# Kernel tuning notes

Hardware: AMD Instinct MI355X
Metric: run time of the kernel (lower is better)

## Reference

```python
import jax, jax.numpy as jnp
import numpy as np
from jax import lax

# Mamba2 block (training path: mamba_split_conv1d_scan_combined equivalent)
B = 2; L = 2048; D_MODEL = 2048
INTER = 4096          # ssm_intermediate_size
NH = 64; HD = INTER // NH   # num_heads, head_dim
N = 128               # ssm_state_size
G = 1                 # n_groups
K = 4                 # conv kernel
CS = 256              # chunk size
EPS = 1e-5
CONV_DIM = INTER + 2 * G * N          # 4352
PROJ_DIM = INTER + CONV_DIM + NH      # 8512


def setup_inputs() -> dict:
    key = jax.random.key(0)
    ks = jax.random.split(key, 4)
    std = 0.02
    return {
        "hidden_states": jax.random.normal(ks[0], (B, L, D_MODEL), jnp.float32),
        "W_in": jax.random.normal(ks[1], (PROJ_DIM, D_MODEL), jnp.float32) * std,
        "conv_w": jax.random.normal(ks[2], (CONV_DIM, K), jnp.float32) * std,
        "conv_b": jnp.zeros((CONV_DIM,), jnp.float32),
        "dt_bias": jnp.ones((NH,), jnp.float32),
        "A_log": jnp.log(jnp.arange(1, NH + 1, dtype=jnp.float32)),
        "D": jnp.ones((NH,), jnp.float32),
        "norm_w": jnp.ones((INTER,), jnp.float32),
        "W_out": jax.random.normal(ks[3], (D_MODEL, INTER), jnp.float32) * std,
    }


def _segsum(x):
    # x: [..., s] -> [..., s, s] lower-triangular cumulative sums (masked with -inf)
    s = x.shape[-1]
    xc = jnp.cumsum(x, axis=-1)
    d = xc[..., :, None] - xc[..., None, :]
    return jnp.where(jnp.tril(jnp.ones((s, s), dtype=bool)), d, -jnp.inf)


def _forward(hidden_states, W_in, conv_w, conv_b, dt_bias, A_log, D, norm_w, W_out):
    proj = hidden_states @ W_in.T                              # [B,L,PROJ_DIM]
    gate = proj[..., :INTER]
    hBC = proj[..., INTER:INTER + CONV_DIM]
    dt = proj[..., INTER + CONV_DIM:]                          # [B,L,NH]

    # causal depthwise conv1d + silu
    xc = hBC.transpose(0, 2, 1)                                # [B,CONV_DIM,L]
    y = lax.conv_general_dilated(
        xc, conv_w[:, None, :], (1,), [(K - 1, 0)],
        dimension_numbers=("NCH", "OIH", "NCH"), feature_group_count=CONV_DIM)
    hBC = jax.nn.silu(y + conv_b[None, :, None]).transpose(0, 2, 1)

    x = hBC[..., :INTER].reshape(B, L, NH, HD)
    Bm = hBC[..., INTER:INTER + G * N].reshape(B, L, G, N)
    Cm = hBC[..., INTER + G * N:].reshape(B, L, G, N)

    dtv = jax.nn.softplus(dt + dt_bias)                        # [B,L,NH], dt_softplus=True
    A = -jnp.exp(A_log)                                        # [NH]

    # ---- chunked selective scan (SSD) ----
    c = L // CS
    xch = x.reshape(B, c, CS, NH, HD)
    dtch = dtv.reshape(B, c, CS, NH)
    Bh = jnp.repeat(Bm.reshape(B, c, CS, G, N), NH // G, axis=3)   # [B,c,s,NH,N]
    Ch = jnp.repeat(Cm.reshape(B, c, CS, G, N), NH // G, axis=3)

    dA = (dtch * A).transpose(0, 3, 1, 2)                      # [B,NH,c,s]
    Acum = jnp.cumsum(dA, axis=-1)                             # [B,NH,c,s]
    Lmat = jnp.exp(_segsum(dA))                                # [B,NH,c,s,s]

    # within-chunk (diagonal block) output
    Ydiag = jnp.einsum("bcihn,bcjhn,bhcij,bcjh,bcjhp->bcihp",
                       Ch, Bh, Lmat, dtch, xch)

    # per-chunk states
    decay_states = jnp.exp(Acum[..., -1:] - Acum)              # [B,NH,c,s]
    states = jnp.einsum("bcjhn,bhcj,bcjh,bcjhp->bchpn",
                        Bh, decay_states, dtch, xch)           # [B,c,NH,HD,N]

    # inter-chunk recurrence (scan over chunks)
    chunk_decay = jnp.exp(Acum[..., -1])                       # [B,NH,c]

    def step(carry, inp):
        st, dec = inp
        new = dec[:, :, None, None] * carry + st
        return new, carry                                      # emit state at chunk start

    init = jnp.zeros((B, NH, HD, N), dtype=x.dtype)
    _, prev = lax.scan(step, init,
                       (states.transpose(1, 0, 2, 3, 4), chunk_decay.transpose(2, 0, 1)))
    prev = prev.transpose(1, 0, 2, 3, 4)                       # [B,c,NH,HD,N]

    Yoff = jnp.einsum("bcihn,bchpn,bhci->bcihp", Ch, prev, jnp.exp(Acum))

    Y = (Ydiag + Yoff).reshape(B, L, NH, HD) + x * D[None, None, :, None]
    yout = Y.reshape(B, L, INTER)

    # gated RMSNorm (norm_before_gate=False): gate first, then normalize
    yout = yout * jax.nn.silu(gate)
    yout = yout * lax.rsqrt(jnp.mean(yout * yout, axis=-1, keepdims=True) + EPS) * norm_w
    return yout @ W_out.T                                      # [B,L,D_MODEL]


def reference(hidden_states, W_in, conv_w, conv_b, dt_bias, A_log, D, norm_w, W_out):
    return _forward(hidden_states, W_in, conv_w, conv_b, dt_bias, A_log, D, norm_w, W_out)
```

## Files before the change

kernel.cpp:

```cpp
#include <hip/hip_runtime.h>
#include <cstdint>

typedef __bf16 bf16;
typedef __bf16 bf16x8 __attribute__((ext_vector_type(8)));
typedef __bf16 bf16x4 __attribute__((ext_vector_type(4)));
typedef float  f32x4  __attribute__((ext_vector_type(4)));

#define BQ     2
#define LQ     2048
#define DMODEL 2048
#define INTER  4096
#define NH     64
#define HD     64
#define NS     128
#define CS     256
#define NC     8
#define CONVD  4352
#define PROJD  8512
#define PROJP  8576
#define PROJW  8704
#define MTOT   4096
#define EPSF   1e-5f
#define LOG2E  1.44269504088896f

__device__ __forceinline__ void async_ld16(const bf16* g, bf16* l) {
  __builtin_amdgcn_global_load_lds(
      (__attribute__((address_space(1))) void*)(uintptr_t)g,
      (__attribute__((address_space(3))) void*)l, 16, 0, 0);
}

__device__ __forceinline__ float siluf(float x) { return x / (1.f + expf(-x)); }

#define SB()    __builtin_amdgcn_sched_barrier(0)
#define HWBAR() __builtin_amdgcn_s_barrier()
#define LGKM0() asm volatile("s_waitcnt lgkmcnt(0)" ::: "memory")

__global__ void cast4_k(const float* __restrict__ in, bf16* __restrict__ out, long n4) {
  long i = (long)blockIdx.x * 256 + threadIdx.x;
  if (i >= n4) return;
  float4 v = ((const float4*)in)[i];
  bf16x4 o; o[0] = (bf16)v.x; o[1] = (bf16)v.y; o[2] = (bf16)v.z; o[3] = (bf16)v.w;
  ((bf16x4*)out)[i] = o;
}

__global__ void cast_pad_win_k(const float* __restrict__ W, bf16* __restrict__ out) {
  long i = (long)blockIdx.x * 256 + threadIdx.x;
  long tot = (long)PROJW * (DMODEL / 4);
  if (i >= tot) return;
  long row = i / (DMODEL / 4);
  long k4  = i % (DMODEL / 4);
  bf16x4 o;
  if (row < PROJD) {
    float4 v = ((const float4*)W)[row * (DMODEL / 4) + k4];
    o[0] = (bf16)v.x; o[1] = (bf16)v.y; o[2] = (bf16)v.z; o[3] = (bf16)v.w;
  } else {
    o[0] = o[1] = o[2] = o[3] = (bf16)0.f;
  }
  ((bf16x4*)out)[i] = o;
}


template<int R0>
__device__ __forceinline__ void ldB4(bf16x8 (&dst)[4][2], const char* base,
                                     int r16, int quad, int xr) {
  #pragma unroll
  for (int f = 0; f < 4; ++f)
    #pragma unroll
    for (int kk = 0; kk < 2; ++kk)
      dst[f][kk] = *(const bf16x8*)(base + (((R0 + f) * 16 + r16) << 7)
                                         + ((((kk << 2) + quad) ^ xr) << 4));
}

template<int R0>
__device__ __forceinline__ void ldA4(bf16x8 (&dst)[8][2], const char* base,
                                     int r16, int quad, int xr) {
  #pragma unroll
  for (int f = 0; f < 4; ++f)
    #pragma unroll
    for (int kk = 0; kk < 2; ++kk)
      dst[R0 + f][kk] = *(const bf16x8*)(base + (((R0 + f) * 16 + r16) << 7)
                                              + ((((kk << 2) + quad) ^ xr) << 4));
}

template<int MH, int NHALF>
__device__ __forceinline__ void qmfma(f32x4 (&acc)[8][4], const bf16x8 (&a)[8][2],
                                      const bf16x8 (&b)[4][2]) {
  #pragma unroll
  for (int kk = 0; kk < 2; ++kk)
    #pragma unroll
    for (int nf = 0; nf < 2; ++nf)
      #pragma unroll
      for (int mm = 0; mm < 4; ++mm)
        acc[MH * 4 + mm][NHALF * 2 + nf] = __builtin_amdgcn_mfma_f32_16x16x32_bf16(
            a[MH * 4 + mm][kk], b[NHALF * 2 + nf][kk], acc[MH * 4 + mm][NHALF * 2 + nf], 0, 0, 0);
}

__global__ __launch_bounds__(512, 2) void gemm8(
    const bf16* __restrict__ A, const bf16* __restrict__ W,
    bf16* __restrict__ Cb, float* __restrict__ Cf,
    int M, int Nn, int Ntiles, int K, int KS, int outf32)
{
  __shared__ int4 lds4[8192];
  char* lds = (char*)lds4;
  const int tid  = threadIdx.x;
  const int w    = tid >> 6;
  const int l    = tid & 63;
  const int wm   = w >> 2;
  const int wn   = w & 3;
  const int quad = l >> 4;
  const int r16  = l & 15;
  const int xr   = r16 & 7;

  const int Mtiles  = M >> 8;
  const int tilesMN = Mtiles * Ntiles;
  const int nwg = tilesMN * KS;
  int bid = blockIdx.x;
  int sid = ((nwg & 7) == 0) ? ((bid & 7) * (nwg >> 3) + (bid >> 3)) : bid;
  const int ks  = sid / tilesMN;
  const int rem = sid - ks * tilesMN;
  const int by = rem % Mtiles;
  const int bx = rem / Mtiles;
  const long tm = (long)by << 8;
  const long tn = (long)bx << 8;
  const int  NT = K / (64 * KS);
  const long kbase = (long)ks * (K / KS);

  const int srow = w * 8 + (l >> 3);
  const int scg  = (l & 7) ^ ((l >> 3) & 7);
  const bf16* Ab = A + (tm + srow) * K + kbase + scg * 8;
  const bf16* Wb = W + (tn + srow) * K + kbase + scg * 8;

  auto stage = [&](int tile, int part) {
    if (tile < NT) {
      const bf16* s = (part < 2 ? Ab : Wb) + (long)((part & 1) * 128) * K + (long)tile * 64;
      char* d = lds + ((tile & 1) << 16) + (part << 14) + (w << 10);
      async_ld16(s, (bf16*)d);
      async_ld16(s + (long)K * 64, (bf16*)(d + 8192));
    }
  };

  stage(0, 0); stage(0, 1); stage(0, 2); stage(0, 3);
  stage(1, 2); stage(1, 3); stage(1, 0);
  asm volatile("s_waitcnt vmcnt(6)" ::: "memory");
  SB();
  HWBAR();

  f32x4 acc[8][4] = {};

  for (int T = 0; T < NT; ++T) {
    const int bsel = (T & 1) << 16;
    const char* as = lds + bsel + (wm << 14);
    const char* bs = lds + bsel + 32768 + ((wn >> 1) << 14) + ((wn & 1) << 13);
    bf16x8 a[8][2], b[4][2];

    ldB4<0>(b, bs, r16, quad, xr);
    ldA4<0>(a, as, r16, quad, xr);
    stage(T + 1, 1);
    HWBAR(); LGKM0(); SB();
    __builtin_amdgcn_s_setprio(1);
    qmfma<0, 0>(acc, a, b);
    __builtin_amdgcn_s_setprio(0);
    HWBAR();

    ldA4<4>(a, as, r16, quad, xr);
    stage(T + 2, 2);
    HWBAR(); LGKM0(); SB();
    __builtin_amdgcn_s_setprio(1);
    qmfma<1, 0>(acc, a, b);
    __builtin_amdgcn_s_setprio(0);
    HWBAR();

    stage(T + 2, 3);
    HWBAR();
    __builtin_amdgcn_s_setprio(1);
    qmfma<0, 1>(acc, a, b);
    __builtin_amdgcn_s_setprio(0);
    HWBAR();

    stage(T + 2, 0);
    HWBAR();
    __builtin_amdgcn_s_setprio(1);
    qmfma<1, 1>(acc, a, b);
    __builtin_amdgcn_s_setprio(0);
    if (T + 2 < NT) { asm volatile("s_waitcnt vmcnt(6)" ::: "memory"); }
    else            { asm volatile("s_waitcnt vmcnt(0)" ::: "memory"); }
    SB();
    HWBAR();
  }

  const long cbase = (long)ks * M * Nn;
  #pragma unroll
  for (int mf = 0; mf < 8; ++mf)
    #pragma unroll
    for (int nf = 0; nf < 4; ++nf) {
      long r0 = tm + wm * 128 + mf * 16 + quad * 4;
      long cc = tn + wn * 64 + nf * 16 + r16;
      if (cc < Nn) {
        #pragma unroll
        for (int reg = 0; reg < 4; ++reg) {
          long idx = (r0 + reg) * (long)Nn + cc;
          if (outf32) Cf[cbase + idx] = acc[mf][nf][reg];
          else        Cb[idx] = (bf16)acc[mf][nf][reg];
        }
      }
    }
}

__global__ void addred_k(const float* __restrict__ P, float* __restrict__ out, long n4) {
  long i = (long)blockIdx.x * 256 + threadIdx.x;
  if (i >= n4) return;
  float4 a = ((const float4*)P)[i];
  float4 b = ((const float4*)P)[i + n4];
  float4 r; r.x = a.x + b.x; r.y = a.y + b.y; r.z = a.z + b.z; r.w = a.w + b.w;
  ((float4*)out)[i] = r;
}

__global__ void conv_silu_k(const bf16* __restrict__ proj,
                            const float* __restrict__ conv_w,
                            const float* __restrict__ conv_b,
                            bf16* __restrict__ xconv,
                            bf16* __restrict__ Bmb, bf16* __restrict__ Cmb,
                            bf16* __restrict__ Bt)
{
  int ch = blockIdx.x * 256 + threadIdx.x;
  if (ch >= CONVD) return;
  long bl = blockIdx.y;
  int l = (int)(bl & (LQ - 1));
  float acc = conv_b[ch];
  #pragma unroll
  for (int t = 0; t < 4; ++t) {
    int ls = l - 3 + t;
    if (ls >= 0)
      acc += (float)proj[(bl - 3 + t) * PROJP + INTER + ch] * conv_w[ch * 4 + t];
  }
  float y = siluf(acc);
  if (ch < INTER) {
    xconv[bl * INTER + ch] = (bf16)y;
  } else if (ch < INTER + NS) {
    int n = ch - INTER;
    Bmb[bl * NS + n] = (bf16)y;
    int b = (int)(bl >> 11), ci = l >> 8, j = l & 255;
    Bt[(((long)(b * NC + ci) * NS) + n) * CS + j] = (bf16)y;
  } else {
    Cmb[bl * NS + (ch - INTER - NS)] = (bf16)y;
  }
}

__global__ __launch_bounds__(CS) void dt_prep_k(
    const bf16* __restrict__ proj, const float* __restrict__ dt_bias,
    const float* __restrict__ A_log,
    float* __restrict__ dtv, float* __restrict__ acum, float* __restrict__ cdec)
{
  int bx = blockIdx.x;
  int ci = bx & 7;
  int bh = bx >> 3;
  int h  = bh & 63;
  int b  = bh >> 6;
  int i  = threadIdx.x;
  long pos = (long)b * LQ + ci * CS + i;
  float draw = (float)proj[pos * PROJP + INTER + CONVD + h] + dt_bias[h];
  float dv = draw > 20.f ? draw : log1pf(expf(draw));
  float Ah = -expf(A_log[h]);
  __shared__ float s[CS];
  s[i] = dv * Ah;
  __syncthreads();
  for (int off = 1; off < CS; off <<= 1) {
    float t = (i >= off) ? s[i - off] : 0.f;
    __syncthreads();
    s[i] += t;
    __syncthreads();
  }
  long base = (long)bx * CS;
  dtv[base + i]  = dv;
  acum[base + i] = s[i];
  if (i == 0) cdec[bx] = expf(s[CS - 1]);
}

__global__ __launch_bounds__(256) void gmat_k(
    const bf16* __restrict__ Cmb, const bf16* __restrict__ Bmb, float* __restrict__ Gnt)
{
  int q  = blockIdx.x;
  int bc = blockIdx.y;
  long bl0 = (long)(bc >> 3) * LQ + (bc & 7) * CS;
  int wave = threadIdx.x >> 6, lane = threadIdx.x & 63;
  int quad = lane >> 4, r16 = lane & 15;
  int i0 = (q >> 1) * 128 + (wave >> 1) * 64;
  int j0 = (q & 1)  * 128 + (wave & 1)  * 64;

  f32x4 acc[4][4] = {};
  #pragma unroll
  for (int kt = 0; kt < 4; ++kt) {
    int k0 = kt * 32 + quad * 8;
    bf16x8 af[4], bfv[4];
    #pragma unroll
    for (int it = 0; it < 4; ++it)
      af[it] = *(const bf16x8*)&Cmb[(bl0 + i0 + it * 16 + r16) * NS + k0];
    #pragma unroll
    for (int nt = 0; nt < 4; ++nt)
      bfv[nt] = *(const bf16x8*)&Bmb[(bl0 + j0 + nt * 16 + r16) * NS + k0];
    #pragma unroll
    for (int it = 0; it < 4; ++it)
      #pragma unroll
      for (int nt = 0; nt < 4; ++nt)
        acc[it][nt] = __builtin_amdgcn_mfma_f32_16x16x32_bf16(af[it], bfv[nt], acc[it][nt], 0, 0, 0);
  }
  #pragma unroll
  for (int it = 0; it < 4; ++it)
    #pragma unroll
    for (int nt = 0; nt < 4; ++nt)
      #pragma unroll
      for (int reg = 0; reg < 4; ++reg) {
        int i = i0 + it * 16 + quad * 4 + reg;
        int j = j0 + nt * 16 + r16;
        Gnt[((long)bc * CS + i) * CS + j] = acc[it][nt][reg];
      }
}

__global__ __launch_bounds__(256) void states_k(
    const bf16* __restrict__ xconv, const bf16* __restrict__ Bt,
    const float* __restrict__ dtv, const float* __restrict__ acum,
    bf16* __restrict__ st)
{
  int bx = blockIdx.x;
  int h = bx & 63, bc = bx >> 6;
  int b = bc >> 3, ci = bc & 7;
  long bl0 = (long)b * LQ + ci * CS;
  long abase = ((long)(b * NH + h) * NC + ci) * CS;
  int t = threadIdx.x;
  int wave = t >> 6, lane = t & 63, quad = lane >> 4, r16 = lane & 15;

  __shared__ bf16 Xt[64][264];
  __shared__ float ws[CS];
  __shared__ float ac_s[CS];
  ac_s[t] = acum[abase + t];
  __syncthreads();
  float alast = ac_s[CS - 1];
  ws[t] = expf(alast - ac_s[t]) * dtv[abase + t];
  {
    int col = t & 63, grp = t >> 6;
    for (int r = 0; r < 64; ++r) {
      int j = grp * 64 + r;
      Xt[col][j] = xconv[(bl0 + j) * INTER + h * HD + col];
    }
  }
  __syncthreads();

  const bf16* btb = &Bt[(long)bc * NS * CS];
  f32x4 acc[8] = {};
  int p = wave * 16 + r16;
  #pragma unroll
  for (int kt = 0; kt < 8; ++kt) {
    int k0 = kt * 32 + quad * 8;
    bf16x8 xv = *(const bf16x8*)&Xt[p][k0];
    float w8[8];
    *(float4*)&w8[0] = *(const float4*)&ws[k0];
    *(float4*)&w8[4] = *(const float4*)&ws[k0 + 4];
    bf16x8 af;
    #pragma unroll
    for (int jj = 0; jj < 8; ++jj) af[jj] = (bf16)((float)xv[jj] * w8[jj]);
    #pragma unroll
    for (int nt = 0; nt < 8; ++nt) {
      bf16x8 bfv = *(const bf16x8*)&btb[(nt * 16 + r16) * CS + k0];
      acc[nt] = __builtin_amdgcn_mfma_f32_16x16x32_bf16(af, bfv, acc[nt], 0, 0, 0);
    }
  }
  #pragma unroll
  for (int nt = 0; nt < 8; ++nt)
    #pragma unroll
    for (int reg = 0; reg < 4; ++reg) {
      int prow = wave * 16 + quad * 4 + reg;
      int n = nt * 16 + r16;
      st[((long)bx * HD + prow) * NS + n] = (bf16)acc[nt][reg];
    }
}

__global__ void scan_k(bf16* __restrict__ st, const float* __restrict__ cdec)
{
  long t = (long)blockIdx.x * 256 + threadIdx.x;
  int n = (int)(t & 127);
  int p = (int)((t >> 7) & 63);
  int h = (int)((t >> 13) & 63);
  int b = (int)(t >> 19);
  float carry = 0.f;
  for (int ci = 0; ci < NC; ++ci) {
    long idx = (((long)(b * NC + ci) * NH + h) * HD + p) * NS + n;
    float v = (float)st[idx];
    st[idx] = (bf16)carry;
    carry = cdec[(b * NH + h) * NC + ci] * carry + v;
  }
}

#define XTP 392
__global__ __launch_bounds__(256) void ymix_k(
    const bf16* __restrict__ xconv, const float* __restrict__ Gnt,
    const bf16* __restrict__ prev, const bf16* __restrict__ Cmb,
    const float* __restrict__ dtv, const float* __restrict__ acum,
    const float* __restrict__ Dp, bf16* __restrict__ Y)
{
  int bx = blockIdx.x;
  int h = bx & 63, bc = bx >> 6;
  int b = bc >> 3, ci = bc & 7;
  long bl0 = (long)b * LQ + ci * CS;
  long abase = ((long)(b * NH + h) * NC + ci) * CS;
  int t = threadIdx.x;
  int wave = t >> 6, lane = t & 63;
  int quad = lane >> 4, r16 = lane & 15;
  int iw = wave * 64;

  __shared__ bf16 Xt[64][XTP];
  __shared__ float a2s[CS], dts[CS], eas[CS];

  {
    float ac = acum[abase + t];
    a2s[t] = ac * LOG2E;
    dts[t] = dtv[abase + t];
    eas[t] = expf(ac);
  }
  {
    int col = t & 63, grp = t >> 6;
    for (int r = 0; r < 64; ++r) {
      int j = grp * 64 + r;
      Xt[col][j] = xconv[(bl0 + j) * INTER + h * HD + col];
    }
  }
  for (int r = 0; r < 32; ++r) {
    int idx = t + r * 256;
    int n = idx & 127, p = idx >> 7;
    Xt[p][256 + n] = prev[((long)bx * HD + p) * NS + n];
  }
  __syncthreads();

  f32x4 acc[4][4] = {};

  for (int kt = 0; kt < 12; ++kt) {
    int k0 = kt * 32;
    bool cpart = (k0 >= 256);
    if (!cpart && k0 > iw + 63) continue;

    bf16x8 bfrag[4];
    #pragma unroll
    for (int nt = 0; nt < 4; ++nt)
      bfrag[nt] = *(const bf16x8*)&Xt[nt * 16 + r16][k0 + quad * 8];

    if (!cpart) {
      int j0 = k0 + quad * 8;
      float dt8[8], a28[8];
      *(float4*)&dt8[0] = *(const float4*)&dts[j0];
      *(float4*)&dt8[4] = *(const float4*)&dts[j0 + 4];
      *(float4*)&a28[0] = *(const float4*)&a2s[j0];
      *(float4*)&a28[4] = *(const float4*)&a2s[j0 + 4];
      #pragma unroll
      for (int it = 0; it < 4; ++it) {
        if (k0 > iw + it * 16 + 15) continue;
        int i = iw + it * 16 + r16;
        float a2i = a2s[i];
        const float* gp = &Gnt[((long)bc * CS + i) * CS + j0];
        float g[8];
        *(float4*)&g[0] = *(const float4*)gp;
        *(float4*)&g[4] = *(const float4*)(gp + 4);
        bf16x8 af;
        #pragma unroll
        for (int jj = 0; jj < 8; ++jj) {
          float v = g[jj] * dt8[jj] * exp2f(a2i - a28[jj]);
          v = (j0 + jj <= i) ? v : 0.f;
          af[jj] = (bf16)v;
        }
        #pragma unroll
        for (int nt = 0; nt < 4; ++nt)
          acc[it][nt] = __builtin_amdgcn_mfma_f32_16x16x32_bf16(af, bfrag[nt], acc[it][nt], 0, 0, 0);
      }
    } else {
      int n0 = k0 - 256 + quad * 8;
      #pragma unroll
      for (int it = 0; it < 4; ++it) {
        int i = iw + it * 16 + r16;
        float e = eas[i];
        bf16x8 cv = *(const bf16x8*)&Cmb[(bl0 + i) * NS + n0];
        bf16x8 af;
        #pragma unroll
        for (int jj = 0; jj < 8; ++jj)
          af[jj] = (bf16)(e * (float)cv[jj]);
        #pragma unroll
        for (int nt = 0; nt < 4; ++nt)
          acc[it][nt] = __builtin_amdgcn_mfma_f32_16x16x32_bf16(af, bfrag[nt], acc[it][nt], 0, 0, 0);
      }
    }
  }

  float Dh = Dp[h];
  #pragma unroll
  for (int it = 0; it < 4; ++it)
    #pragma unroll
    for (int nt = 0; nt < 4; ++nt) {
      int i0 = iw + it * 16 + quad * 4;
      int p  = nt * 16 + r16;
      bf16x4 xv = *(const bf16x4*)&Xt[p][i0];
      #pragma unroll
      for (int reg = 0; reg < 4; ++reg) {
        float v = acc[it][nt][reg] + Dh * (float)xv[reg];
        Y[(bl0 + i0 + reg) * INTER + h * HD + p] = (bf16)v;
      }
    }
}

__global__ __launch_bounds__(256) void norm_k(
    bf16* __restrict__ Y, const bf16* __restrict__ proj,
    const float* __restrict__ norm_w)
{
  long bl = blockIdx.x;
  int t = threadIdx.x;
  __shared__ float yb[INTER];
  __shared__ float red[256];
  float ss = 0.f;
  for (int r = 0; r < 16; ++r) {
    int ch = t + r * 256;
    float g = (float)proj[bl * PROJP + ch];
    float yv = (float)Y[bl * INTER + ch] * siluf(g);
    yb[ch] = yv;
    ss += yv * yv;
  }
  red[t] = ss;
  __syncthreads();
  for (int s = 128; s > 0; s >>= 1) {
    if (t < s) red[t] += red[t + s];
    __syncthreads();
  }
  float scale = rsqrtf(red[0] / (float)INTER + EPSF);
  for (int r = 0; r < 16; ++r) {
    int ch = t + r * 256;
    Y[bl * INTER + ch] = (bf16)(yb[ch] * scale * norm_w[ch]);
  }
}

extern "C" void kernel_launch(void* const* d_in, const int* in_sizes, int n_in,
                              void* d_out, int out_size, void* d_ws, size_t ws_size,
                              hipStream_t stream)
{
  (void)in_sizes; (void)n_in; (void)out_size; (void)ws_size;
  const float* hidden  = (const float*)d_in[0];
  const float* W_in    = (const float*)d_in[1];
  const float* conv_w  = (const float*)d_in[2];
  const float* conv_b  = (const float*)d_in[3];
  const float* dt_bias = (const float*)d_in[4];
  const float* A_log   = (const float*)d_in[5];
  const float* Dp      = (const float*)d_in[6];
  const float* norm_w  = (const float*)d_in[7];
  const float* W_out   = (const float*)d_in[8];
  float* out = (float*)d_out;

  char* ws    = (char*)d_ws;
  bf16* projb = (bf16*)(ws);
  char* base2 = ws + 70254592;
  bf16*  hb    = (bf16*)(base2);
  bf16*  winb  = (bf16*)(base2 + 16777216);
  bf16*  xconv = (bf16*)(base2);
  bf16*  st    = (bf16*)(base2 + 33554432);
  float* Gnt   = (float*)(base2 + 50331648);
  bf16*  Bmb   = (bf16*)(base2 + 54525952);
  bf16*  Cmb   = (bf16*)(base2 + 55574528);
  float* dtv   = (float*)(base2 + 56623104);
  float* acum  = (float*)(base2 + 57671680);
  float* cdec  = (float*)(base2 + 58720256);
  bf16*  Bt    = (bf16*)(base2 + 58724352);
  bf16*  Yb    = xconv;
  bf16*  woutb = st;

  cast4_k<<<dim3((unsigned)((MTOT * (long)DMODEL / 4 + 255) / 256)), 256, 0, stream>>>(
      hidden, hb, (long)MTOT * DMODEL / 4);
  cast_pad_win_k<<<dim3((unsigned)(((long)PROJW * (DMODEL / 4) + 255) / 256)), 256, 0, stream>>>(
      W_in, winb);
  gemm8<<<dim3((PROJW / 256) * (MTOT / 256)), 512, 0, stream>>>(
      hb, winb, projb, nullptr, MTOT, PROJP, PROJW / 256, DMODEL, 1, 0);

  conv_silu_k<<<dim3(CONVD / 256, MTOT), 256, 0, stream>>>(
      projb, conv_w, conv_b, xconv, Bmb, Cmb, Bt);
  dt_prep_k<<<dim3(BQ * NH * NC), CS, 0, stream>>>(
      projb, dt_bias, A_log, dtv, acum, cdec);
  gmat_k<<<dim3(4, BQ * NC), 256, 0, stream>>>(Cmb, Bmb, Gnt);
  states_k<<<dim3(BQ * NC * NH), 256, 0, stream>>>(xconv, Bt, dtv, acum, st);
  scan_k<<<dim3(BQ * NH * HD * NS / 256), 256, 0, stream>>>(st, cdec);
  ymix_k<<<dim3(BQ * NC * NH), 256, 0, stream>>>(
      xconv, Gnt, st, Cmb, dtv, acum, Dp, Yb);

  cast4_k<<<dim3((unsigned)((DMODEL * (long)INTER / 4 + 255) / 256)), 256, 0, stream>>>(
      W_out, woutb, (long)DMODEL * INTER / 4);
  norm_k<<<dim3(MTOT), 256, 0, stream>>>(Yb, projb, norm_w);
  gemm8<<<dim3((DMODEL / 256) * (MTOT / 256) * 2), 512, 0, stream>>>(
      Yb, woutb, nullptr, (float*)projb, MTOT, DMODEL, DMODEL / 256, INTER, 2, 1);
  addred_k<<<dim3((unsigned)((MTOT * (long)DMODEL / 4 + 255) / 256)), 256, 0, stream>>>(
      (const float*)projb, out, (long)MTOT * DMODEL / 4);
}
```

Baseline: 667.9 us.

## Restructure GEMM main loop into half-tile register double buffering; vectorize norm kernel

```diff
diff --git a/kernel.cpp b/kernel.cpp
--- a/kernel.cpp
+++ b/kernel.cpp
@@ -33,7 +33,6 @@
 
 #define SB()    __builtin_amdgcn_sched_barrier(0)
 #define HWBAR() __builtin_amdgcn_s_barrier()
-#define LGKM0() asm volatile("s_waitcnt lgkmcnt(0)" ::: "memory")
 
 __global__ void cast4_k(const float* __restrict__ in, bf16* __restrict__ out, long n4) {
   long i = (long)blockIdx.x * 256 + threadIdx.x;
@@ -60,39 +59,39 @@
 }
 
 
-template<int R0>
-__device__ __forceinline__ void ldB4(bf16x8 (&dst)[4][2], const char* base,
+template<int MH>
+__device__ __forceinline__ void ldAh(bf16x8 (&dst)[4][2], const char* base,
                                      int r16, int quad, int xr) {
   #pragma unroll
   for (int f = 0; f < 4; ++f)
     #pragma unroll
     for (int kk = 0; kk < 2; ++kk)
-      dst[f][kk] = *(const bf16x8*)(base + (((R0 + f) * 16 + r16) << 7)
+      dst[f][kk] = *(const bf16x8*)(base + ((((MH * 4 + f) * 16) + r16) << 7)
                                          + ((((kk << 2) + quad) ^ xr) << 4));
 }
 
-template<int R0>
-__device__ __forceinline__ void ldA4(bf16x8 (&dst)[8][2], const char* base,
+template<int NH2>
+__device__ __forceinline__ void ldBh(bf16x8 (&dst)[2][2], const char* base,
                                      int r16, int quad, int xr) {
   #pragma unroll
-  for (int f = 0; f < 4; ++f)
+  for (int f = 0; f < 2; ++f)
     #pragma unroll
     for (int kk = 0; kk < 2; ++kk)
-      dst[R0 + f][kk] = *(const bf16x8*)(base + (((R0 + f) * 16 + r16) << 7)
-                                              + ((((kk << 2) + quad) ^ xr) << 4));
-}
-
-template<int MH, int NHALF>
-__device__ __forceinline__ void qmfma(f32x4 (&acc)[8][4], const bf16x8 (&a)[8][2],
-                                      const bf16x8 (&b)[4][2]) {
+      dst[f][kk] = *(const bf16x8*)(base + ((((NH2 * 2 + f) * 16) + r16) << 7)
+                                         + ((((kk << 2) + quad) ^ xr) << 4));
+}
+
+template<int MH, int NH2>
+__device__ __forceinline__ void qmfma(f32x4 (&acc)[8][4], const bf16x8 (&a)[4][2],
+                                      const bf16x8 (&b)[2][2]) {
   #pragma unroll
   for (int kk = 0; kk < 2; ++kk)
     #pragma unroll
     for (int nf = 0; nf < 2; ++nf)
       #pragma unroll
       for (int mm = 0; mm < 4; ++mm)
-        acc[MH * 4 + mm][NHALF * 2 + nf] = __builtin_amdgcn_mfma_f32_16x16x32_bf16(
-            a[MH * 4 + mm][kk], b[NHALF * 2 + nf][kk], acc[MH * 4 + mm][NHALF * 2 + nf], 0, 0, 0);
+        acc[MH * 4 + mm][NH2 * 2 + nf] = __builtin_amdgcn_mfma_f32_16x16x32_bf16(
+            a[mm][kk], b[nf][kk], acc[MH * 4 + mm][NH2 * 2 + nf], 0, 0, 0);
 }
 
 __global__ __launch_bounds__(512, 2) void gemm8(
@@ -140,53 +139,56 @@
   };
 
   stage(0, 0); stage(0, 1); stage(0, 2); stage(0, 3);
-  stage(1, 2); stage(1, 3); stage(1, 0);
-  asm volatile("s_waitcnt vmcnt(6)" ::: "memory");
+  stage(1, 2); stage(1, 3);
+  asm volatile("s_waitcnt vmcnt(4)" ::: "memory");
   SB();
   HWBAR();
+  SB();
+
+  bf16x8 a0[4][2], a1[4][2], b0[2][2], b1[2][2];
+  {
+    const char* as0 = lds + (wm << 14);
+    const char* bs0 = lds + 32768 + ((wn >> 1) << 14) + ((wn & 1) << 13);
+    ldAh<0>(a0, as0, r16, quad, xr);
+    ldBh<0>(b0, bs0, r16, quad, xr);
+  }
 
   f32x4 acc[8][4] = {};
 
   for (int T = 0; T < NT; ++T) {
-    const int bsel = (T & 1) << 16;
-    const char* as = lds + bsel + (wm << 14);
-    const char* bs = lds + bsel + 32768 + ((wn >> 1) << 14) + ((wn & 1) << 13);
-    bf16x8 a[8][2], b[4][2];
-
-    ldB4<0>(b, bs, r16, quad, xr);
-    ldA4<0>(a, as, r16, quad, xr);
-    stage(T + 1, 1);
-    HWBAR(); LGKM0(); SB();
+    const int bsel  = (T & 1) << 16;
+    const char* as  = lds + bsel + (wm << 14);
+    const char* bs  = lds + bsel + 32768 + ((wn >> 1) << 14) + ((wn & 1) << 13);
+    const char* asN = lds + (bsel ^ 0x10000) + (wm << 14);
+    const char* bsN = lds + (bsel ^ 0x10000) + 32768 + ((wn >> 1) << 14) + ((wn & 1) << 13);
+
+    SB();
+    stage(T + 1, 0); stage(T + 1, 1);
+    ldBh<1>(b1, bs, r16, quad, xr);
+    ldAh<1>(a1, as, r16, quad, xr);
+    SB(); HWBAR(); SB();
+
     __builtin_amdgcn_s_setprio(1);
-    qmfma<0, 0>(acc, a, b);
+    qmfma<0, 0>(acc, a0, b0);
     __builtin_amdgcn_s_setprio(0);
-    HWBAR();
-
-    ldA4<4>(a, as, r16, quad, xr);
-    stage(T + 2, 2);
-    HWBAR(); LGKM0(); SB();
+    SB(); HWBAR(); SB();
+
     __builtin_amdgcn_s_setprio(1);
-    qmfma<1, 0>(acc, a, b);
+    qmfma<0, 1>(acc, a0, b1);
     __builtin_amdgcn_s_setprio(0);
-    HWBAR();
-
-    stage(T + 2, 3);
-    HWBAR();
+    asm volatile("s_waitcnt vmcnt(0)" ::: "memory");
+    SB(); HWBAR(); SB();
+
     __builtin_amdgcn_s_setprio(1);
-    qmfma<0, 1>(acc, a, b);
+    qmfma<1, 0>(acc, a1, b0);
+    qmfma<1, 1>(acc, a1, b1);
     __builtin_amdgcn_s_setprio(0);
-    HWBAR();
-
-    stage(T + 2, 0);
-    HWBAR();
-    __builtin_amdgcn_s_setprio(1);
-    qmfma<1, 1>(acc, a, b);
-    __builtin_amdgcn_s_setprio(0);
-    if (T + 2 < NT) { asm volatile("s_waitcnt vmcnt(6)" ::: "memory"); }
-    else            { asm volatile("s_waitcnt vmcnt(0)" ::: "memory"); }
-    SB();
-    HWBAR();
-  }
+    ldAh<0>(a0, asN, r16, quad, xr);
+    ldBh<0>(b0, bsN, r16, quad, xr);
+    stage(T + 2, 2); stage(T + 2, 3);
+    SB(); HWBAR();
+  }
+  asm volatile("s_waitcnt vmcnt(0)" ::: "memory");
 
   const long cbase = (long)ks * M * Nn;
   #pragma unroll
@@ -509,16 +511,31 @@
 {
   long bl = blockIdx.x;
   int t = threadIdx.x;
-  __shared__ float yb[INTER];
+  const bf16* yrow = Y + bl * INTER;
+  const bf16* grow = proj + bl * PROJP;
+  int c0 = t * 16;
+
+  bf16x8 y0 = *(const bf16x8*)&yrow[c0];
+  bf16x8 y1 = *(const bf16x8*)&yrow[c0 + 8];
+  bf16x8 g0 = *(const bf16x8*)&grow[c0];
+  bf16x8 g1 = *(const bf16x8*)&grow[c0 + 8];
+
+  float yv[16];
+  float ss = 0.f;
+  #pragma unroll
+  for (int j = 0; j < 8; ++j) {
+    float g = (float)g0[j];
+    float v = (float)y0[j] * (g / (1.f + expf(-g)));
+    yv[j] = v; ss += v * v;
+  }
+  #pragma unroll
+  for (int j = 0; j < 8; ++j) {
+    float g = (float)g1[j];
+    float v = (float)y1[j] * (g / (1.f + expf(-g)));
+    yv[8 + j] = v; ss += v * v;
+  }
+
   __shared__ float red[256];
-  float ss = 0.f;
-  for (int r = 0; r < 16; ++r) {
-    int ch = t + r * 256;
-    float g = (float)proj[bl * PROJP + ch];
-    float yv = (float)Y[bl * INTER + ch] * siluf(g);
-    yb[ch] = yv;
-    ss += yv * yv;
-  }
   red[t] = ss;
   __syncthreads();
   for (int s = 128; s > 0; s >>= 1) {
@@ -526,10 +543,22 @@
     __syncthreads();
   }
   float scale = rsqrtf(red[0] / (float)INTER + EPSF);
-  for (int r = 0; r < 16; ++r) {
-    int ch = t + r * 256;
-    Y[bl * INTER + ch] = (bf16)(yb[ch] * scale * norm_w[ch]);
-  }
+
+  float4 w0 = *(const float4*)&norm_w[c0];
+  float4 w1 = *(const float4*)&norm_w[c0 + 4];
+  float4 w2 = *(const float4*)&norm_w[c0 + 8];
+  float4 w3 = *(const float4*)&norm_w[c0 + 12];
+  float wv[16];
+  *(float4*)&wv[0] = w0; *(float4*)&wv[4] = w1;
+  *(float4*)&wv[8] = w2; *(float4*)&wv[12] = w3;
+
+  bf16x8 o0, o1;
+  #pragma unroll
+  for (int j = 0; j < 8; ++j) o0[j] = (bf16)(yv[j] * scale * wv[j]);
+  #pragma unroll
+  for (int j = 0; j < 8; ++j) o1[j] = (bf16)(yv[8 + j] * scale * wv[8 + j]);
+  *(bf16x8*)&Y[bl * INTER + c0]     = o0;
+  *(bf16x8*)&Y[bl * INTER + c0 + 8] = o1;
 }
 
 extern "C" void kernel_launch(void* const* d_in, const int* in_sizes, int n_in,
```

New measurement: 644.2 us. 1.04x faster.
